# Optimization experiments

Hardware: AMD Instinct MI355X
Metric: run time of the kernel (lower is better)

The kernel has to match this reference:

```python
import jax, jax.numpy as jnp
from jax import lax
import numpy as np

UNITS, S, B, T = 64, 16, 512, 4096
LOG_2PI = float(np.log(2.0 * np.pi))


def setup_inputs() -> dict:
    key = jax.random.key(0)
    k1, k2 = jax.random.split(key)
    inputs = jax.random.normal(k1, (B, T), dtype=jnp.float32)
    # positive 'probs' (TFP Categorical takes log internally)
    hmm_params = jax.random.uniform(k2, (UNITS, S, S), dtype=jnp.float32,
                                    minval=1e-3, maxval=1.0)
    return {"inputs": inputs, "hmm_params": hmm_params}


def reference(inputs, hmm_params):
    # --- HMM parameters, as TFP builds them ---
    trans = hmm_params[0]                      # (S, S) unnormalized probs
    log_A = jnp.log(trans) - jnp.log(trans.sum(-1, keepdims=True))  # (S,S) row-normalized
    init = hmm_params[0, 0]                    # (S,)
    log_pi = jnp.log(init) - jnp.log(init.sum())
    # Emission: Normal(loc=0, scale=1) per state -> same logp for every state
    emit = -0.5 * inputs * inputs - 0.5 * LOG_2PI   # [B, T]
    emit = emit[:, :, None]                          # [B, T, 1] broadcasts over S

    # --- Viterbi forward (max-product) ---
    delta0 = log_pi[None, :] + emit[:, 0]            # [B, S]
    emit_seq = jnp.moveaxis(emit[:, 1:], 1, 0)       # [T-1, B, 1]

    def step(delta, e_t):
        scores = delta[:, :, None] + log_A[None, :, :]   # [B, S_prev, S_cur]
        psi = jnp.argmax(scores, axis=1).astype(jnp.int32)  # [B, S]
        delta_new = jnp.max(scores, axis=1) + e_t            # [B, S]
        return delta_new, psi

    deltaT, psis = lax.scan(step, delta0, emit_seq)  # psis: [T-1, B, S]

    # --- Backtrace ---
    zT = jnp.argmax(deltaT, axis=-1).astype(jnp.int32)   # [B]

    def back(z, psi):
        z_prev = jnp.take_along_axis(psi, z[:, None], axis=1)[:, 0]
        return z_prev, z_prev

    _, zs = lax.scan(back, zT, psis, reverse=True)   # zs: [T-1, B] = states t=0..T-2
    path = jnp.concatenate([zs.T, zT[:, None]], axis=1)  # [B, T]
    return path
```

## Files before the change

kernel.cpp:

```cpp
#include <hip/hip_runtime.h>
#include <math.h>

#define T_LEN 4096
#define B_SZ  512

__device__ __forceinline__ float emis(float xv) {
    float a = __fmul_rn(-0.5f, xv);
    float b = __fmul_rn(a, xv);
    return __fsub_rn(b, (float)0.9189385332046727);
}

__global__ __launch_bounds__(256) void k_emit(const float* __restrict__ x,
                                              float* __restrict__ Epad,
                                              float* __restrict__ E0,
                                              const float* __restrict__ hmm,
                                              float* __restrict__ logA,
                                              float* __restrict__ logAT) {
    int tid = threadIdx.x;
    if (blockIdx.x == 0) {
        int i = tid >> 4, j = tid & 15;
        const float* row = hmm + i * 16;
        float r[8];
#pragma unroll
        for (int k = 0; k < 8; ++k) r[k] = __fadd_rn(row[k], row[k + 8]);
        float s = __fadd_rn(
            __fadd_rn(__fadd_rn(r[0], r[1]), __fadd_rn(r[2], r[3])),
            __fadd_rn(__fadd_rn(r[4], r[5]), __fadd_rn(r[6], r[7])));
        float la = (float)log((double)row[j]);
        float ls = (float)log((double)s);
        float v = __fsub_rn(la, ls);
        logA[tid] = v;
        logAT[j * 16 + i] = v;
    }
    int i = blockIdx.x * 256 + tid;
    const float4* x4 = (const float4*)x;
    float4 xa = x4[i];
    float4 xb = (i + 1 < (B_SZ * T_LEN / 4)) ? x4[i + 1] : xa;
    float4 e;
    e.x = emis(xa.y); e.y = emis(xa.z); e.z = emis(xa.w); e.w = emis(xb.x);
    ((float4*)Epad)[i] = e;
    if ((i & 1023) == 0) E0[i >> 10] = emis(xa.x);
}

#define DPP_ROR0(K, SRC) __builtin_amdgcn_update_dpp(0, (SRC), 0x120 + (K), 0xF, 0xF, false)
#define M3(x, y, z) fmaxf(fmaxf(x, y), z)

#define ADDPP(DST, K)                                                                 \
    asm("v_add_f32_dpp %0, %1, %2 row_ror:" #K " row_mask:0xf bank_mask:0xf"          \
        : "=v"(DST) : "v"(d), "v"(a[K]))

#define STEPC(ET)                                                                     \
    {                                                                                 \
        float s0 = __fadd_rn(d, a[0]);                                                \
        float s1, s2, s3, s4, s5, s6, s7, s8, s9, s10, s11, s12, s13, s14, s15;       \
        ADDPP(s1, 1);   ADDPP(s2, 2);   ADDPP(s3, 3);   ADDPP(s4, 4);                 \
        ADDPP(s5, 5);   ADDPP(s6, 6);   ADDPP(s7, 7);   ADDPP(s8, 8);                 \
        ADDPP(s9, 9);   ADDPP(s10, 10); ADDPP(s11, 11); ADDPP(s12, 12);               \
        ADDPP(s13, 13); ADDPP(s14, 14); ADDPP(s15, 15);                               \
        float u0 = M3(s0, s1, s2),  u1 = M3(s3, s4, s5),  u2 = M3(s6, s7, s8);        \
        float u3 = M3(s9, s10, s11), u4 = M3(s12, s13, s14);                          \
        float m = fmaxf(M3(u0, u1, u2), M3(u3, u4, s15));                             \
        d = __fadd_rn(m, ET);                                                         \
    }

#define GRP4(QV, SLOTDW)                                                              \
    {                                                                                 \
        float4 dq;                                                                    \
        STEPC(QV.x) dq.x = d; STEPC(QV.y) dq.y = d;                                   \
        STEPC(QV.z) dq.z = d; STEPC(QV.w) dq.w = d;                                   \
        *(float4*)(db + (SLOTDW)) = dq;                                               \
    }

#define PERMSEL(V, Q)                                                                 \
    {                                                                                 \
        int sel_ = (V) & 7;                                                           \
        int lo_, hi_;                                                                 \
        asm("v_perm_b32 %0, %1, %2, %3" : "=v"(lo_) : "v"((Q).y), "v"((Q).x), "v"(sel_)); \
        asm("v_perm_b32 %0, %1, %2, %3" : "=v"(hi_) : "v"((Q).w), "v"((Q).z), "v"(sel_)); \
        V = (((V) & 8) ? hi_ : lo_) & 0xff;                                           \
    }

#define WALK64(BASE, CUR, PRE, POST)                                                  \
    {                                                                                 \
        uint4 m_[8];                                                                  \
        _Pragma("unroll") for (int z_ = 0; z_ < 8; ++z_)                              \
            m_[z_] = *(const uint4*)((BASE) + (63 - z_) * 16);                        \
        for (int r_ = 63; r_ >= 15; r_ -= 8) {                                        \
            uint4 n_[8];                                                              \
            _Pragma("unroll") for (int z_ = 0; z_ < 8; ++z_)                          \
                n_[z_] = *(const uint4*)((BASE) + (r_ - 8 - z_) * 16);                \
            _Pragma("unroll") for (int z_ = 0; z_ < 8; ++z_) {                        \
                PRE(r_ - z_, CUR) PERMSEL(CUR, m_[z_]) POST(r_ - z_, CUR)             \
            }                                                                         \
            _Pragma("unroll") for (int z_ = 0; z_ < 8; ++z_) m_[z_] = n_[z_];         \
        }                                                                             \
        _Pragma("unroll") for (int z_ = 0; z_ < 8; ++z_) {                            \
            PRE(7 - z_, CUR) PERMSEL(CUR, m_[z_]) POST(7 - z_, CUR)                   \
        }                                                                             \
    }

#define NIBHOP(V, Q) (V) = (int)(((Q) >> ((unsigned)(V) << 2)) & 15ull);

#define NWALK64(BASE, CUR, POST)                                                      \
    {                                                                                 \
        const unsigned long long* bb_ = (BASE);                                       \
        unsigned long long m_[8];                                                     \
        _Pragma("unroll") for (int z_ = 0; z_ < 8; ++z_) m_[z_] = bb_[63 - z_];       \
        for (int r_ = 63; r_ >= 15; r_ -= 8) {                                       \
            unsigned long long n_[8];                                                 \
            _Pragma("unroll") for (int z_ = 0; z_ < 8; ++z_) n_[z_] = bb_[r_ - 8 - z_]; \
            _Pragma("unroll") for (int z_ = 0; z_ < 8; ++z_) {                        \
                NIBHOP(CUR, m_[z_]) POST(r_ - z_, CUR)                                \
            }                                                                         \
            _Pragma("unroll") for (int z_ = 0; z_ < 8; ++z_) m_[z_] = n_[z_];         \
        }                                                                             \
        _Pragma("unroll") for (int z_ = 0; z_ < 8; ++z_) {                            \
            NIBHOP(CUR, m_[z_]) POST(7 - z_, CUR)                                     \
        }                                                                             \
    }

#define NOPX(r, c)
#define EBL_PRE(r, c) eb[r] = (unsigned char)(c);
#define OUT_POST(r, c) ob[r] = (c);

__global__ __launch_bounds__(256) void k_main(const float* __restrict__ Epad,
                                              const float* __restrict__ E0,
                                              const float* __restrict__ logA,
                                              const float* __restrict__ logAT,
                                              int* __restrict__ out) {
    __shared__ __align__(16) float dbuf[2][2][16][68];
    __shared__ unsigned long long pnib[2][64 * 65];
    __shared__ uint4 Mlv[2][64];
    __shared__ unsigned char Ebl[2][64];
    __shared__ float carry_l[2][16];
    const int tid = threadIdx.x;
    const int wave = tid >> 6;
    const int blk = blockIdx.x;

    if (wave == 0) {
        asm volatile("s_setprio 3");
        const int j = tid & 15, g = tid >> 4;
        float a[16];
        float d = 0.f;
        float4 q0, q1, q2, q3;
        const float4* ep4 = nullptr;
        if (g < 2) {
            int b = blk * 2 + g;
            a[0] = logA[j * 16 + j];
#define LOADA(K) { int sk = DPP_ROR0(K, j); a[K] = logA[sk * 16 + j]; }
            LOADA(1)  LOADA(2)  LOADA(3)  LOADA(4)  LOADA(5)
            LOADA(6)  LOADA(7)  LOADA(8)  LOADA(9)  LOADA(10)
            LOADA(11) LOADA(12) LOADA(13) LOADA(14) LOADA(15)
#undef LOADA
            ep4 = (const float4*)(Epad + (size_t)b * T_LEN);
            d = __fadd_rn(logA[j], E0[b]);
            q0 = ep4[0]; q1 = ep4[1]; q2 = ep4[2]; q3 = ep4[3];
        }
        for (int p = 0; p < 66; ++p) {
            __syncthreads();
            if (p < 64 && g < 2) {
                float* db = &dbuf[p & 1][g][j][0];
                db[64] = d;
                const float4* epc = ep4 + 16 * p;
                if (p < 63) {
#pragma clang loop unroll(disable)
                    for (int ii = 0; ii < 4; ++ii) {
                        GRP4(q0, ii * 16 + 0)  q0 = epc[(ii + 1) * 4 + 0];
                        GRP4(q1, ii * 16 + 4)  q1 = epc[(ii + 1) * 4 + 1];
                        GRP4(q2, ii * 16 + 8)  q2 = epc[(ii + 1) * 4 + 2];
                        GRP4(q3, ii * 16 + 12) q3 = epc[(ii + 1) * 4 + 3];
                    }
                } else {
#pragma clang loop unroll(disable)
                    for (int ii = 0; ii < 3; ++ii) {
                        GRP4(q0, ii * 16 + 0)  q0 = epc[(ii + 1) * 4 + 0];
                        GRP4(q1, ii * 16 + 4)  q1 = epc[(ii + 1) * 4 + 1];
                        GRP4(q2, ii * 16 + 8)  q2 = epc[(ii + 1) * 4 + 2];
                        GRP4(q3, ii * 16 + 12) q3 = epc[(ii + 1) * 4 + 3];
                    }
                    GRP4(q0, 48) GRP4(q1, 52) GRP4(q2, 56)
                    STEPC(q3.x) db[60] = d;
                    STEPC(q3.y) db[61] = d;
                    STEPC(q3.z) db[62] = d;
                }
            }
        }
        if (g < 2) carry_l[g][j] = d;
    } else if (wave <= 2) {
        const int g2 = wave - 1;
        const int r = tid & 63;
        for (int p = 0; p < 66; ++p) {
            __syncthreads();
            const int c = p - 1;
            if (c >= 0 && c < 64) {
                const int t2 = 64 * c + 1 + r;
                if (t2 <= T_LEN - 1) {
                    const int q = c & 1;
                    const int rs = (r == 0) ? 64 : (r - 1);
                    float dd[16];
#pragma unroll
                    for (int i = 0; i < 16; ++i) dd[i] = dbuf[q][g2][i][rs];
                    unsigned long long pk = 0ull;
#pragma clang loop unroll(disable)
                    for (int jj = 0; jj < 16; ++jj) {
                        const float* col = logAT + (jj << 4);
                        float best = __fadd_rn(dd[0], col[0]);
                        int arg = 0;
#pragma unroll
                        for (int i = 1; i < 16; ++i) {
                            float s = __fadd_rn(dd[i], col[i]);
                            if (s > best) arg = i;
                            best = fmaxf(best, s);
                        }
                        pk |= (unsigned long long)arg << (jj * 4);
                    }
                    pnib[g2][c * 65 + r] = pk;
                } else {
                    pnib[g2][c * 65 + 63] = 0xFEDCBA9876543210ull;
                }
            }
        }
    } else {
        const int l = tid - 192;
        const int g3 = l >> 4, z = l & 15;
        for (int p = 0; p < 66; ++p) {
            __syncthreads();
            const int c = p - 2;
            if (c >= 0 && l < 32) {
                int cur = z;
                NWALK64(&pnib[g3][c * 65], cur, NOPX)
                ((unsigned char*)&Mlv[g3][c])[z] = (unsigned char)cur;
            }
        }
    }

    __syncthreads();
    if (tid < 2) {
        const int g = tid;
        float best = carry_l[g][0]; int zT = 0;
#pragma unroll
        for (int i = 1; i < 16; ++i) {
            float s = carry_l[g][i];
            if (s > best) zT = i;
            best = fmaxf(best, s);
        }
        int z = zT;
        unsigned char* eb = &Ebl[g][0];
        WALK64((const unsigned char*)&Mlv[g][0], z, EBL_PRE, NOPX)
    }
    __syncthreads();
    if (tid < 128) {
        const int g = tid >> 6, c = tid & 63;
        int* ob = out + (size_t)(blk * 2 + g) * T_LEN + c * 64;
        int cur = Ebl[g][c];
        NWALK64(&pnib[g][c * 65], cur, OUT_POST)
    }
}

extern "C" void kernel_launch(void* const* d_in, const int* in_sizes, int n_in,
                              void* d_out, int out_size, void* d_ws, size_t ws_size,
                              hipStream_t stream) {
    (void)in_sizes; (void)n_in; (void)out_size; (void)ws_size;
    const float* x   = (const float*)d_in[0];
    const float* hmm = (const float*)d_in[1];
    int* out = (int*)d_out;

    char* w = (char*)d_ws;
    float* logA  = (float*)w;
    float* logAT = (float*)(w + 1024);
    float* E0    = (float*)(w + 2048);
    float* Epad  = (float*)(w + 4096);

    hipLaunchKernelGGL(k_emit, dim3((B_SZ * T_LEN / 4) / 256), dim3(256), 0, stream,
                       x, Epad, E0, hmm, logA, logAT);

    hipLaunchKernelGGL(k_main, dim3(B_SZ / 2), dim3(256), 0, stream,
                       Epad, E0, logA, logAT, out);
}
```

Baseline: 305.7 us.

## Fuse emission and log-transition prep into main Viterbi kernel via LDS ring

Removes the separate emission kernel and its workspace round-trip. Each block now computes log-normalized transitions into shared memory, and the backtrace wave produces emissions into a 4-deep LDS ring two chunks ahead of the forward wave. The argmax waves read transition columns from LDS as float4 with register prefetch instead of from global memory. This saves one launch and a full global write and read of the emission array, at the cost of redundant per-block log computation and extra work on the walker wave.

```diff
diff --git a/kernel.cpp b/kernel.cpp
--- a/kernel.cpp
+++ b/kernel.cpp
@@ -8,38 +8,6 @@
     float a = __fmul_rn(-0.5f, xv);
     float b = __fmul_rn(a, xv);
     return __fsub_rn(b, (float)0.9189385332046727);
-}
-
-__global__ __launch_bounds__(256) void k_emit(const float* __restrict__ x,
-                                              float* __restrict__ Epad,
-                                              float* __restrict__ E0,
-                                              const float* __restrict__ hmm,
-                                              float* __restrict__ logA,
-                                              float* __restrict__ logAT) {
-    int tid = threadIdx.x;
-    if (blockIdx.x == 0) {
-        int i = tid >> 4, j = tid & 15;
-        const float* row = hmm + i * 16;
-        float r[8];
-#pragma unroll
-        for (int k = 0; k < 8; ++k) r[k] = __fadd_rn(row[k], row[k + 8]);
-        float s = __fadd_rn(
-            __fadd_rn(__fadd_rn(r[0], r[1]), __fadd_rn(r[2], r[3])),
-            __fadd_rn(__fadd_rn(r[4], r[5]), __fadd_rn(r[6], r[7])));
-        float la = (float)log((double)row[j]);
-        float ls = (float)log((double)s);
-        float v = __fsub_rn(la, ls);
-        logA[tid] = v;
-        logAT[j * 16 + i] = v;
-    }
-    int i = blockIdx.x * 256 + tid;
-    const float4* x4 = (const float4*)x;
-    float4 xa = x4[i];
-    float4 xb = (i + 1 < (B_SZ * T_LEN / 4)) ? x4[i + 1] : xa;
-    float4 e;
-    e.x = emis(xa.y); e.y = emis(xa.z); e.z = emis(xa.w); e.w = emis(xb.x);
-    ((float4*)Epad)[i] = e;
-    if ((i & 1023) == 0) E0[i >> 10] = emis(xa.x);
 }
 
 #define DPP_ROR0(K, SRC) __builtin_amdgcn_update_dpp(0, (SRC), 0x120 + (K), 0xF, 0xF, false)
@@ -123,19 +91,41 @@
 #define EBL_PRE(r, c) eb[r] = (unsigned char)(c);
 #define OUT_POST(r, c) ob[r] = (c);
 
-__global__ __launch_bounds__(256) void k_main(const float* __restrict__ Epad,
-                                              const float* __restrict__ E0,
-                                              const float* __restrict__ logA,
-                                              const float* __restrict__ logAT,
-                                              int* __restrict__ out) {
+__global__ __launch_bounds__(256) void k_fused(const float* __restrict__ x,
+                                               const float* __restrict__ hmm,
+                                               int* __restrict__ out) {
     __shared__ __align__(16) float dbuf[2][2][16][68];
     __shared__ unsigned long long pnib[2][64 * 65];
     __shared__ uint4 Mlv[2][64];
     __shared__ unsigned char Ebl[2][64];
     __shared__ float carry_l[2][16];
+    __shared__ float logA_l[256];
+    __shared__ __align__(16) float logAT_l[272];
+    __shared__ __align__(16) float Ebuf[4][2][64];
+
     const int tid = threadIdx.x;
     const int wave = tid >> 6;
     const int blk = blockIdx.x;
+
+    {
+        const int i = tid >> 4, j = tid & 15;
+        const float* row = hmm + i * 16;
+        float r[8];
+#pragma unroll
+        for (int k = 0; k < 8; ++k) r[k] = __fadd_rn(row[k], row[k + 8]);
+        float s = __fadd_rn(
+            __fadd_rn(__fadd_rn(r[0], r[1]), __fadd_rn(r[2], r[3])),
+            __fadd_rn(__fadd_rn(r[4], r[5]), __fadd_rn(r[6], r[7])));
+        float la = (float)log((double)row[j]);
+        float ls = (float)log((double)s);
+        float v = __fsub_rn(la, ls);
+        logA_l[tid] = v;
+        logAT_l[j * 16 + i] = v;
+        if (tid < 16) logAT_l[256 + tid] = 0.f;
+        const int cc0 = tid >> 7, gp = (tid >> 6) & 1, l0 = tid & 63;
+        Ebuf[cc0][gp][l0] = emis(x[(size_t)(blk * 2 + gp) * T_LEN + 64 * cc0 + l0 + 1]);
+    }
+    __syncthreads();
 
     if (wave == 0) {
         asm volatile("s_setprio 3");
@@ -143,40 +133,45 @@
         float a[16];
         float d = 0.f;
         float4 q0, q1, q2, q3;
-        const float4* ep4 = nullptr;
         if (g < 2) {
-            int b = blk * 2 + g;
-            a[0] = logA[j * 16 + j];
-#define LOADA(K) { int sk = DPP_ROR0(K, j); a[K] = logA[sk * 16 + j]; }
+            const int b = blk * 2 + g;
+            a[0] = logA_l[j * 16 + j];
+#define LOADA(K) { int sk = DPP_ROR0(K, j); a[K] = logA_l[sk * 16 + j]; }
             LOADA(1)  LOADA(2)  LOADA(3)  LOADA(4)  LOADA(5)
             LOADA(6)  LOADA(7)  LOADA(8)  LOADA(9)  LOADA(10)
             LOADA(11) LOADA(12) LOADA(13) LOADA(14) LOADA(15)
 #undef LOADA
-            ep4 = (const float4*)(Epad + (size_t)b * T_LEN);
-            d = __fadd_rn(logA[j], E0[b]);
-            q0 = ep4[0]; q1 = ep4[1]; q2 = ep4[2]; q3 = ep4[3];
+            float e0 = emis(x[(size_t)b * T_LEN]);
+            d = __fadd_rn(logA_l[j], e0);
+            const float4* e0p = (const float4*)&Ebuf[0][g][0];
+            q0 = e0p[0]; q1 = e0p[1]; q2 = e0p[2]; q3 = e0p[3];
         }
         for (int p = 0; p < 66; ++p) {
             __syncthreads();
             if (p < 64 && g < 2) {
                 float* db = &dbuf[p & 1][g][j][0];
                 db[64] = d;
-                const float4* epc = ep4 + 16 * p;
+                const float4* ecur = (const float4*)&Ebuf[p & 3][g][0];
+                const float4* enxt = (const float4*)&Ebuf[(p + 1) & 3][g][0];
                 if (p < 63) {
 #pragma clang loop unroll(disable)
-                    for (int ii = 0; ii < 4; ++ii) {
-                        GRP4(q0, ii * 16 + 0)  q0 = epc[(ii + 1) * 4 + 0];
-                        GRP4(q1, ii * 16 + 4)  q1 = epc[(ii + 1) * 4 + 1];
-                        GRP4(q2, ii * 16 + 8)  q2 = epc[(ii + 1) * 4 + 2];
-                        GRP4(q3, ii * 16 + 12) q3 = epc[(ii + 1) * 4 + 3];
+                    for (int ii = 0; ii < 3; ++ii) {
+                        GRP4(q0, ii * 16 + 0)  q0 = ecur[(ii + 1) * 4 + 0];
+                        GRP4(q1, ii * 16 + 4)  q1 = ecur[(ii + 1) * 4 + 1];
+                        GRP4(q2, ii * 16 + 8)  q2 = ecur[(ii + 1) * 4 + 2];
+                        GRP4(q3, ii * 16 + 12) q3 = ecur[(ii + 1) * 4 + 3];
                     }
+                    GRP4(q0, 48) q0 = enxt[0];
+                    GRP4(q1, 52) q1 = enxt[1];
+                    GRP4(q2, 56) q2 = enxt[2];
+                    GRP4(q3, 60) q3 = enxt[3];
                 } else {
 #pragma clang loop unroll(disable)
                     for (int ii = 0; ii < 3; ++ii) {
-                        GRP4(q0, ii * 16 + 0)  q0 = epc[(ii + 1) * 4 + 0];
-                        GRP4(q1, ii * 16 + 4)  q1 = epc[(ii + 1) * 4 + 1];
-                        GRP4(q2, ii * 16 + 8)  q2 = epc[(ii + 1) * 4 + 2];
-                        GRP4(q3, ii * 16 + 12) q3 = epc[(ii + 1) * 4 + 3];
+                        GRP4(q0, ii * 16 + 0)  q0 = ecur[(ii + 1) * 4 + 0];
+                        GRP4(q1, ii * 16 + 4)  q1 = ecur[(ii + 1) * 4 + 1];
+                        GRP4(q2, ii * 16 + 8)  q2 = ecur[(ii + 1) * 4 + 2];
+                        GRP4(q3, ii * 16 + 12) q3 = ecur[(ii + 1) * 4 + 3];
                     }
                     GRP4(q0, 48) GRP4(q1, 52) GRP4(q2, 56)
                     STEPC(q3.x) db[60] = d;
@@ -201,18 +196,22 @@
 #pragma unroll
                     for (int i = 0; i < 16; ++i) dd[i] = dbuf[q][g2][i][rs];
                     unsigned long long pk = 0ull;
+                    const float4* clp = (const float4*)&logAT_l[0];
+                    float4 c0 = clp[0], c1 = clp[1], c2 = clp[2], c3 = clp[3];
 #pragma clang loop unroll(disable)
                     for (int jj = 0; jj < 16; ++jj) {
-                        const float* col = logAT + (jj << 4);
-                        float best = __fadd_rn(dd[0], col[0]);
+                        const float4* nxp = clp + ((jj + 1) << 2);
+                        float4 n0 = nxp[0], n1 = nxp[1], n2 = nxp[2], n3 = nxp[3];
+                        float best = __fadd_rn(dd[0], c0.x);
                         int arg = 0;
-#pragma unroll
-                        for (int i = 1; i < 16; ++i) {
-                            float s = __fadd_rn(dd[i], col[i]);
-                            if (s > best) arg = i;
-                            best = fmaxf(best, s);
-                        }
+#define PSI1(IDX, COMP) { float s_ = __fadd_rn(dd[IDX], COMP); if (s_ > best) arg = IDX; best = fmaxf(best, s_); }
+                        PSI1(1, c0.y)  PSI1(2, c0.z)  PSI1(3, c0.w)
+                        PSI1(4, c1.x)  PSI1(5, c1.y)  PSI1(6, c1.z)  PSI1(7, c1.w)
+                        PSI1(8, c2.x)  PSI1(9, c2.y)  PSI1(10, c2.z) PSI1(11, c2.w)
+                        PSI1(12, c3.x) PSI1(13, c3.y) PSI1(14, c3.z) PSI1(15, c3.w)
+#undef PSI1
                         pk |= (unsigned long long)arg << (jj * 4);
+                        c0 = n0; c1 = n1; c2 = n2; c3 = n3;
                     }
                     pnib[g2][c * 65 + r] = pk;
                 } else {
@@ -225,6 +224,14 @@
         const int g3 = l >> 4, z = l & 15;
         for (int p = 0; p < 66; ++p) {
             __syncthreads();
+            const int cc = p + 2;
+            if (cc < 64) {
+                const int t = 64 * cc + l + 1;
+                if (t <= T_LEN - 1) {
+                    Ebuf[cc & 3][0][l] = emis(x[(size_t)(blk * 2 + 0) * T_LEN + t]);
+                    Ebuf[cc & 3][1][l] = emis(x[(size_t)(blk * 2 + 1) * T_LEN + t]);
+                }
+            }
             const int c = p - 2;
             if (c >= 0 && l < 32) {
                 int cur = z;
@@ -260,20 +267,10 @@
 extern "C" void kernel_launch(void* const* d_in, const int* in_sizes, int n_in,
                               void* d_out, int out_size, void* d_ws, size_t ws_size,
                               hipStream_t stream) {
-    (void)in_sizes; (void)n_in; (void)out_size; (void)ws_size;
+    (void)in_sizes; (void)n_in; (void)out_size; (void)d_ws; (void)ws_size;
     const float* x   = (const float*)d_in[0];
     const float* hmm = (const float*)d_in[1];
     int* out = (int*)d_out;
 
-    char* w = (char*)d_ws;
-    float* logA  = (float*)w;
-    float* logAT = (float*)(w + 1024);
-    float* E0    = (float*)(w + 2048);
-    float* Epad  = (float*)(w + 4096);
-
-    hipLaunchKernelGGL(k_emit, dim3((B_SZ * T_LEN / 4) / 256), dim3(256), 0, stream,
-                       x, Epad, E0, hmm, logA, logAT);
-
-    hipLaunchKernelGGL(k_main, dim3(B_SZ / 2), dim3(256), 0, stream,
-                       Epad, E0, logA, logAT, out);
+    hipLaunchKernelGGL(k_fused, dim3(B_SZ / 2), dim3(256), 0, stream, x, hmm, out);
 }
```

After: 295.2 us. 3.4% less time.
